# Optimization experiments

Measured on AMD Instinct MI355X. Metric: run time of the kernel, lower is better.

## Reference

```python
import jax, jax.numpy as jnp
import numpy as np

STATE_LEN = 128
SEQ_LEN = 2048  # middle segment length; total T = SEQ_LEN + 2*STATE_LEN = 2304


def _l2norm(t):
    # matches torch F.normalize(p=2, dim=-1, eps=1e-12)
    n = jnp.sqrt(jnp.sum(t * t, axis=-1, keepdims=True))
    return t / jnp.maximum(n, 1e-12)


def setup_inputs() -> dict:
    key = jax.random.key(0)
    ks = jax.random.split(key, 8)
    B, D, H, dk, dv = 1, 1024, 16, 64, 64
    T = SEQ_LEN + 2 * STATE_LEN
    x = jax.random.normal(ks[0], (B, T, D), dtype=jnp.float32)
    w = lambda k, do: jax.random.normal(k, (H, D, do), dtype=jnp.float32) * 0.02
    return {
        "x": x,
        "Wq": w(ks[1], dk),
        "Wk": w(ks[2], dk),
        "Wv": w(ks[3], dv),
        "Wq_state": w(ks[4], dk),
        "Wk_state": w(ks[5], dk),
        "Wv_state": w(ks[6], dv),
        "scaling_factor": jnp.full((H,), 1.0 / np.sqrt(dk), dtype=jnp.float32),
    }


def reference(x, Wq, Wk, Wv, Wq_state, Wk_state, Wv_state, scaling_factor):
    sl, seq = STATE_LEN, SEQ_LEN
    # extract_state: [start_state | sequence | end_state]
    x0 = x[:, :sl]
    xm = x[:, sl:sl + seq]
    x1 = x[:, sl + seq:]

    proj = lambda t, W: jnp.einsum('bsd,hdk->bhsk', t, W)  # StackedLinear, no bias

    q = jnp.concatenate([_l2norm(proj(x0, Wq_state)), _l2norm(proj(xm, Wq)), _l2norm(proj(x1, Wq_state))], axis=2)
    k = jnp.concatenate([_l2norm(proj(x0, Wk_state)), _l2norm(proj(xm, Wk)), _l2norm(proj(x1, Wk_state))], axis=2)
    v = jnp.concatenate([_l2norm(proj(x0, Wv_state)), _l2norm(proj(xm, Wv)), _l2norm(proj(x1, Wv_state))], axis=2)

    T = q.shape[2]
    row = jnp.arange(T)[:, None]
    col = jnp.arange(T)[None, :]
    allowed = col <= row  # causal (tril, diagonal=0)
    # end-state rows may not attend to start-state cols (attn_bias[..., seq+sl:seq+2sl, :sl] = 0 before log)
    allowed = allowed & ~((row >= sl + seq) & (col < sl))
    mask = jnp.where(allowed, 0.0, -jnp.inf).astype(q.dtype)  # log of 0/1 tril

    # per-head learnable scale applied to q@k^T, then additive mask, softmax, @v
    scores = jnp.einsum('bhqd,bhkd->bhqk', q, k) * scaling_factor[None, :, None, None] + mask
    att = jax.nn.softmax(scores, axis=-1)
    return jnp.einsum('bhqk,bhkd->bhqd', att, v)
```

## Files before the change

kernel.cpp:

```cpp
#include <hip/hip_runtime.h>
#include <hip/hip_bf16.h>

#define T_TOT 2304
#define DDIM  1024
#define NH    16
#define DK    64
#define SLEN  128
#define SEQ   2048

typedef __bf16 bf16x8 __attribute__((ext_vector_type(8)));
typedef __bf16 bf16x4 __attribute__((ext_vector_type(4)));
typedef float  f32x4  __attribute__((ext_vector_type(4)));
typedef float  f32x16 __attribute__((ext_vector_type(16)));

__device__ __forceinline__ void async_copy16(const void* gsrc, void* ldst) {
  __builtin_amdgcn_global_load_lds(
      (const __attribute__((address_space(1))) void*)gsrc,
      (__attribute__((address_space(3))) void*)ldst, 16, 0, 0);
}

__device__ __forceinline__ void lds_barrier() {
  __asm__ volatile("s_waitcnt lgkmcnt(0)\n\ts_barrier" ::: "memory");
}

__global__ __launch_bounds__(256) void convert_kernel(
    const float* __restrict__ x,
    const float* __restrict__ Wq, const float* __restrict__ Wk,
    const float* __restrict__ Wv, const float* __restrict__ Wqs,
    const float* __restrict__ Wks, const float* __restrict__ Wvs,
    __bf16* __restrict__ xb, __bf16* __restrict__ Wt) {
  const int b = blockIdx.x;
  const int tid = threadIdx.x;
  if (b < 576) {
    const float4* xin = (const float4*)x;
#pragma unroll
    for (int it = 0; it < 4; ++it) {
      int idx4 = b * 1024 + it * 256 + tid;
      float4 v = xin[idx4];
      bf16x4 o;
      o[0] = (__bf16)v.x; o[1] = (__bf16)v.y; o[2] = (__bf16)v.z; o[3] = (__bf16)v.w;
      *(bf16x4*)(xb + (size_t)idx4 * 4) = o;
    }
    return;
  }
  __shared__ float tile[64 * 65];
  const int wb = b - 576;
  const int m  = wb >> 8;
  const int rem = wb & 255;
  const int h  = rem >> 4;
  const int dt = rem & 15;
  const int d0 = dt * 64;
  const float* Wsrc = (m == 0 ? Wq : m == 1 ? Wk : m == 2 ? Wv
                      : m == 3 ? Wqs : m == 4 ? Wks : Wvs) + (size_t)h * (DDIM * DK);
#pragma unroll
  for (int rr = 0; rr < 4; ++rr) {
    int drow = rr * 16 + (tid >> 4);
    int nc   = (tid & 15) * 4;
    float4 v = *(const float4*)(Wsrc + (size_t)(d0 + drow) * DK + nc);
    tile[(nc + 0) * 65 + drow] = v.x;
    tile[(nc + 1) * 65 + drow] = v.y;
    tile[(nc + 2) * 65 + drow] = v.z;
    tile[(nc + 3) * 65 + drow] = v.w;
  }
  __syncthreads();
  {
    int n  = tid >> 2;
    int rg = (tid & 3) * 16;
    __bf16* dst = Wt + (((size_t)(m * NH + h)) * DK + n) * DDIM + d0 + rg;
    bf16x8 o0, o1;
#pragma unroll
    for (int e = 0; e < 8; e++) o0[e] = (__bf16)tile[n * 65 + rg + e];
#pragma unroll
    for (int e = 0; e < 8; e++) o1[e] = (__bf16)tile[n * 65 + rg + 8 + e];
    *(bf16x8*)dst = o0;
    *(bf16x8*)(dst + 8) = o1;
  }
}

__global__ __launch_bounds__(256) void proj_kernel(
    const __bf16* __restrict__ xb, const __bf16* __restrict__ Wt,
    const float* __restrict__ scal,
    __bf16* __restrict__ qkv, __bf16* __restrict__ vt) {
  const int ntile = blockIdx.x;
  const int rt    = blockIdx.y;
  const int which = blockIdx.z;
  const int r0    = rt * 128;
  const int m     = (rt == 0 || rt == 17) ? which + 3 : which;

  __shared__ __bf16 Xs[128 * 64];
  __shared__ __bf16 Wsh[128 * 64];

  const int tid  = threadIdx.x;
  const int wave = tid >> 6, lane = tid & 63;
  const int quad = lane >> 4, lc = lane & 15;
  const int wr   = wave >> 1, wc = wave & 1;
  const int h    = ntile * 2 + wc;

  const __bf16* Wbase = Wt + ((size_t)m * NH) * (DK * DDIM) + (size_t)(ntile * 128) * DDIM;

  const f32x4 fz = {0.f, 0.f, 0.f, 0.f};
  f32x4 acc[4][4];
#pragma unroll
  for (int i = 0; i < 4; i++)
#pragma unroll
    for (int j = 0; j < 4; j++) acc[i][j] = fz;

  for (int k0 = 0; k0 < DDIM; k0 += 64) {
#pragma unroll
    for (int it = 0; it < 4; ++it) {
      int L = it * 256 + tid;
      int row = L >> 3, c = (L & 7) ^ ((L >> 3) & 7);
      async_copy16(xb + (size_t)(r0 + row) * DDIM + k0 + c * 8,
                   (char*)Xs + (size_t)(it * 256 + wave * 64) * 16);
    }
#pragma unroll
    for (int it = 0; it < 4; ++it) {
      int L = it * 256 + tid;
      int row = L >> 3, c = (L & 7) ^ ((L >> 3) & 7);
      async_copy16(Wbase + (size_t)row * DDIM + k0 + c * 8,
                   (char*)Wsh + (size_t)(it * 256 + wave * 64) * 16);
    }
    __syncthreads();
#pragma unroll
    for (int kk = 0; kk < 2; kk++) {
      bf16x8 afr[4], bfr[4];
#pragma unroll
      for (int i = 0; i < 4; i++) {
        int row = wr * 64 + i * 16 + lc;
        int ch  = (kk * 4 + quad) ^ (row & 7);
        afr[i] = *(const bf16x8*)(Xs + (row * 8 + ch) * 8);
      }
#pragma unroll
      for (int j = 0; j < 4; j++) {
        int row = wc * 64 + j * 16 + lc;
        int ch  = (kk * 4 + quad) ^ (row & 7);
        bfr[j] = *(const bf16x8*)(Wsh + (row * 8 + ch) * 8);
      }
#pragma unroll
      for (int i = 0; i < 4; i++)
#pragma unroll
        for (int j = 0; j < 4; j++)
          acc[i][j] = __builtin_amdgcn_mfma_f32_16x16x32_bf16(afr[i], bfr[j], acc[i][j], 0, 0, 0);
    }
    __syncthreads();
  }

  const float qscale = (which == 0) ? scal[h] * 1.44269504088896f : 1.0f;
  float inv4[4][4];
#pragma unroll
  for (int i = 0; i < 4; i++) {
#pragma unroll
    for (int r = 0; r < 4; r++) {
      float s = 0.f;
#pragma unroll
      for (int j = 0; j < 4; j++) { float v = acc[i][j][r]; s += v * v; }
#pragma unroll
      for (int off = 1; off < 16; off <<= 1) s += __shfl_xor(s, off, 64);
      inv4[i][r] = qscale / fmaxf(sqrtf(s), 1e-12f);
    }
  }
  if (which == 2) {
    __bf16* vtp = vt + (size_t)h * (DK * T_TOT);
#pragma unroll
    for (int i = 0; i < 4; i++) {
      int rowbase = r0 + wr * 64 + i * 16 + quad * 4;
#pragma unroll
      for (int j = 0; j < 4; j++) {
        bf16x4 o;
#pragma unroll
        for (int r = 0; r < 4; r++) o[r] = (__bf16)(acc[i][j][r] * inv4[i][r]);
        *(bf16x4*)(vtp + (size_t)(j * 16 + lc) * T_TOT + rowbase) = o;
      }
    }
  } else {
    __bf16* outp = qkv + ((size_t)(which * NH + h)) * ((size_t)T_TOT * DK);
#pragma unroll
    for (int i = 0; i < 4; i++)
#pragma unroll
      for (int r = 0; r < 4; r++) {
        int row = r0 + wr * 64 + i * 16 + quad * 4 + r;
#pragma unroll
        for (int j = 0; j < 4; j++)
          outp[(size_t)row * DK + j * 16 + lc] = (__bf16)(acc[i][j][r] * inv4[i][r]);
      }
  }
}

__global__ __launch_bounds__(256, 3) void attn_kernel(
    const __bf16* __restrict__ qkv, const __bf16* __restrict__ vt,
    float* __restrict__ out) {
  const int b    = blockIdx.x;
  const int h    = b & 15;
  const int qg   = 35 - (b >> 4);
  const int q0b  = qg * 64;
  const int tid  = threadIdx.x;
  const int wave = tid >> 6, lane = tid & 63;
  const int quad = lane >> 4, lc = lane & 15;
  const int l32  = lane & 31, hi = lane >> 5;

  const __bf16* qp = qkv + ((size_t)h) * ((size_t)T_TOT * DK);
  const __bf16* kp = qkv + ((size_t)(NH + h)) * ((size_t)T_TOT * DK);
  const __bf16* vp = vt + (size_t)h * (DK * T_TOT);

  __shared__ __bf16 Ks[2][64 * 64];
  __shared__ __bf16 Vs[2][64 * 64];
  __shared__ __bf16 Ps[64 * 64];
  __shared__ float  lred[4][64];

  bf16x8 qf[4][2];
#pragma unroll
  for (int qt = 0; qt < 4; qt++)
#pragma unroll
    for (int kk = 0; kk < 2; kk++)
      qf[qt][kk] = *(const bf16x8*)(qp + (size_t)(q0b + qt * 16 + lc) * DK + kk * 32 + quad * 8);

  f32x16 acc_o;
#pragma unroll
  for (int e = 0; e < 16; e++) acc_o[e] = 0.f;
  float lp[4] = {0.f, 0.f, 0.f, 0.f};

  const int jstart = (q0b >= SLEN + SEQ) ? 2 : 0;
  const int jend   = qg;

  auto stage = [&](int j, int bufi) {
    const __bf16* kT = kp + (size_t)j * 64 * DK;
#pragma unroll
    for (int it = 0; it < 2; ++it) {
      int L = it * 256 + tid;
      int row = L >> 3, c = (L & 7) ^ ((L >> 3) & 7);
      async_copy16(kT + (size_t)row * DK + c * 8,
                   (char*)&Ks[bufi][0] + (size_t)(it * 256 + wave * 64) * 16);
    }
#pragma unroll
    for (int it = 0; it < 2; ++it) {
      int L = it * 256 + tid;
      int d = L >> 3, c = (L & 7) ^ ((L >> 3) & 7);
      async_copy16(vp + (size_t)d * T_TOT + j * 64 + c * 8,
                   (char*)&Vs[bufi][0] + (size_t)(it * 256 + wave * 64) * 16);
    }
  };

  stage(jstart, 0);
  int cur = 0;

  const int d0 = (wave >> 1) * 32;
  const int q0 = (wave & 1) * 32;

  for (int j = jstart; j <= jend; ++j) {
    __syncthreads();
    if (j < jend) stage(j + 1, cur ^ 1);

    const bool diag = (j == jend);

    bf16x8 kA[2];
#pragma unroll
    for (int kk = 0; kk < 2; kk++) {
      int row = wave * 16 + lc;
      kA[kk] = *(const bf16x8*)(&Ks[cur][(row * 8 + ((kk * 4 + quad) ^ (lc & 7))) * 8]);
    }
    f32x4 s[4];
#pragma unroll
    for (int qt = 0; qt < 4; qt++) {
      s[qt] = (f32x4){0.f, 0.f, 0.f, 0.f};
#pragma unroll
      for (int kk = 0; kk < 2; kk++)
        s[qt] = __builtin_amdgcn_mfma_f32_16x16x32_bf16(kA[kk], qf[qt][kk], s[qt], 0, 0, 0);
    }

#pragma unroll
    for (int qt = 0; qt < 4; qt++) {
      if (diag) {
#pragma unroll
        for (int r = 0; r < 4; r++)
          if ((wave * 16 + quad * 4 + r) > (qt * 16 + lc)) s[qt][r] = -__builtin_inff();
      }
      bf16x4 pb;
#pragma unroll
      for (int r = 0; r < 4; r++) {
        float pe = exp2f(s[qt][r]);
        lp[qt] += pe;
        pb[r] = (__bf16)pe;
      }
      int el = (qt * 16 + lc) * 64 + (((wave * 2 + (quad >> 1)) ^ (lc & 7)) * 8) + (quad & 1) * 4;
      *(bf16x4*)(&Ps[el]) = pb;
    }

    lds_barrier();

#pragma unroll
    for (int ks = 0; ks < 4; ks++) {
      int ch = (ks * 2 + hi) ^ (l32 & 7);
      bf16x8 vA = *(const bf16x8*)(&Vs[cur][((d0 + l32) * 8 + ch) * 8]);
      bf16x8 pB = *(const bf16x8*)(&Ps[((q0 + l32) * 8 + ch) * 8]);
      acc_o = __builtin_amdgcn_mfma_f32_32x32x16_bf16(vA, pB, acc_o, 0, 0, 0);
    }
    cur ^= 1;
  }

#pragma unroll
  for (int qt = 0; qt < 4; qt++) {
    lp[qt] += __shfl_xor(lp[qt], 16, 64);
    lp[qt] += __shfl_xor(lp[qt], 32, 64);
  }
  lred[wave][quad * 16 + lc] = lp[quad];
  __syncthreads();
  float lsum = lred[0][q0 + l32] + lred[1][q0 + l32] + lred[2][q0 + l32] + lred[3][q0 + l32];
  float invl = 1.0f / lsum;

  const size_t rowbase = ((size_t)h * T_TOT + q0b + q0 + l32) * DK;
#pragma unroll
  for (int g = 0; g < 4; g++) {
    f32x4 o;
#pragma unroll
    for (int t = 0; t < 4; t++) o[t] = acc_o[g * 4 + t] * invl;
    *(f32x4*)(&out[rowbase + d0 + 4 * hi + 8 * g]) = o;
  }
}

extern "C" void kernel_launch(void* const* d_in, const int* in_sizes, int n_in,
                              void* d_out, int out_size, void* d_ws, size_t ws_size,
                              hipStream_t stream) {
  const float* x    = (const float*)d_in[0];
  const float* Wq   = (const float*)d_in[1];
  const float* Wk   = (const float*)d_in[2];
  const float* Wv   = (const float*)d_in[3];
  const float* Wqs  = (const float*)d_in[4];
  const float* Wks  = (const float*)d_in[5];
  const float* Wvs  = (const float*)d_in[6];
  const float* scal = (const float*)d_in[7];
  float* out = (float*)d_out;

  char* ws = (char*)d_ws;
  size_t off = 0;
  __bf16* xb  = (__bf16*)(ws + off); off += (size_t)T_TOT * DDIM * 2;
  __bf16* Wt  = (__bf16*)(ws + off); off += (size_t)6 * NH * DK * DDIM * 2;
  __bf16* qkv = (__bf16*)(ws + off); off += (size_t)2 * NH * T_TOT * DK * 2;
  __bf16* vt  = (__bf16*)(ws + off);

  convert_kernel<<<2112, 256, 0, stream>>>(x, Wq, Wk, Wv, Wqs, Wks, Wvs, xb, Wt);
  proj_kernel<<<dim3(8, 18, 3), 256, 0, stream>>>(xb, Wt, scal, qkv, vt);
  attn_kernel<<<dim3(576), 256, 0, stream>>>(qkv, vt, out);
}
```

Before: 155.7 us.

## Split attention key range across two blocks and add combine kernel

Each query tile's causal key range is split into two halves processed by separate blocks, which write unnormalized partial outputs and row sums to workspace. A new combine kernel sums the two partials and normalizes. This doubles the grid and shortens the longest per-block loop to reduce causal load imbalance. In exchange it adds partial-result memory traffic and an extra kernel launch.

New measurement: 148.5 us. 1.05x faster.

```diff
diff --git a/kernel.cpp b/kernel.cpp
--- a/kernel.cpp
+++ b/kernel.cpp
@@ -188,10 +188,12 @@
 
 __global__ __launch_bounds__(256, 3) void attn_kernel(
     const __bf16* __restrict__ qkv, const __bf16* __restrict__ vt,
-    float* __restrict__ out) {
+    float* __restrict__ Opart, float* __restrict__ Lpart) {
   const int b    = blockIdx.x;
   const int h    = b & 15;
-  const int qg   = 35 - (b >> 4);
+  const int rest = b >> 4;
+  const int qg   = 35 - (rest >> 1);
+  const int si   = rest & 1;
   const int q0b  = qg * 64;
   const int tid  = threadIdx.x;
   const int wave = tid >> 6, lane = tid & 63;
@@ -219,8 +221,11 @@
   for (int e = 0; e < 16; e++) acc_o[e] = 0.f;
   float lp[4] = {0.f, 0.f, 0.f, 0.f};
 
-  const int jstart = (q0b >= SLEN + SEQ) ? 2 : 0;
-  const int jend   = qg;
+  const int jsAll = (q0b >= SLEN + SEQ) ? 2 : 0;
+  const int n     = qg - jsAll + 1;
+  const int half  = (n + 1) >> 1;
+  const int j0    = jsAll + (si ? half : 0);
+  const int j1    = si ? qg : (jsAll + half - 1);
 
   auto stage = [&](int j, int bufi) {
     const __bf16* kT = kp + (size_t)j * 64 * DK;
@@ -240,17 +245,17 @@
     }
   };
 
-  stage(jstart, 0);
   int cur = 0;
+  if (j0 <= j1) stage(j0, 0);
 
   const int d0 = (wave >> 1) * 32;
   const int q0 = (wave & 1) * 32;
 
-  for (int j = jstart; j <= jend; ++j) {
+  for (int j = j0; j <= j1; ++j) {
     __syncthreads();
-    if (j < jend) stage(j + 1, cur ^ 1);
-
-    const bool diag = (j == jend);
+    if (j < j1) stage(j + 1, cur ^ 1);
+
+    const bool diag = (j == qg);
 
     bf16x8 kA[2];
 #pragma unroll
@@ -304,16 +309,48 @@
   }
   lred[wave][quad * 16 + lc] = lp[quad];
   __syncthreads();
-  float lsum = lred[0][q0 + l32] + lred[1][q0 + l32] + lred[2][q0 + l32] + lred[3][q0 + l32];
-  float invl = 1.0f / lsum;
-
-  const size_t rowbase = ((size_t)h * T_TOT + q0b + q0 + l32) * DK;
+  if (wave == 0)
+    Lpart[(size_t)b * 64 + lane] = lred[0][lane] + lred[1][lane] + lred[2][lane] + lred[3][lane];
+
+  float* Ob = Opart + (size_t)b * 4096;
+  const size_t rowbase = (size_t)(q0 + l32) * DK;
 #pragma unroll
   for (int g = 0; g < 4; g++) {
     f32x4 o;
 #pragma unroll
-    for (int t = 0; t < 4; t++) o[t] = acc_o[g * 4 + t] * invl;
-    *(f32x4*)(&out[rowbase + d0 + 4 * hi + 8 * g]) = o;
+    for (int t = 0; t < 4; t++) o[t] = acc_o[g * 4 + t];
+    *(f32x4*)(&Ob[rowbase + d0 + 4 * hi + 8 * g]) = o;
+  }
+}
+
+__global__ __launch_bounds__(256) void combine_kernel(
+    const float* __restrict__ Opart, const float* __restrict__ Lpart,
+    float* __restrict__ out) {
+  const int b  = blockIdx.x;
+  const int h  = b & 15;
+  const int qg = b >> 4;
+  const int b0 = (((35 - qg) * 2) << 4) | h;
+  const int b1 = b0 + 16;
+  const int tid = threadIdx.x;
+
+  __shared__ float invl[64];
+  if (tid < 64)
+    invl[tid] = 1.0f / (Lpart[(size_t)b0 * 64 + tid] + Lpart[(size_t)b1 * 64 + tid]);
+  __syncthreads();
+
+  const float* O0 = Opart + (size_t)b0 * 4096;
+  const float* O1 = Opart + (size_t)b1 * 4096;
+  float* op = out + ((size_t)h * T_TOT + qg * 64) * DK;
+#pragma unroll
+  for (int it = 0; it < 4; ++it) {
+    int i4 = it * 256 + tid;
+    f32x4 a = *(const f32x4*)(&O0[i4 * 4]);
+    f32x4 c = *(const f32x4*)(&O1[i4 * 4]);
+    float iv = invl[i4 >> 4];
+    f32x4 o;
+#pragma unroll
+    for (int r = 0; r < 4; r++) o[r] = (a[r] + c[r]) * iv;
+    *(f32x4*)(&op[i4 * 4]) = o;
   }
 }
 
@@ -332,12 +369,15 @@
 
   char* ws = (char*)d_ws;
   size_t off = 0;
-  __bf16* xb  = (__bf16*)(ws + off); off += (size_t)T_TOT * DDIM * 2;
-  __bf16* Wt  = (__bf16*)(ws + off); off += (size_t)6 * NH * DK * DDIM * 2;
-  __bf16* qkv = (__bf16*)(ws + off); off += (size_t)2 * NH * T_TOT * DK * 2;
-  __bf16* vt  = (__bf16*)(ws + off);
+  __bf16* xb    = (__bf16*)(ws + off); off += (size_t)T_TOT * DDIM * 2;
+  __bf16* Wt    = (__bf16*)(ws + off); off += (size_t)6 * NH * DK * DDIM * 2;
+  __bf16* qkv   = (__bf16*)(ws + off); off += (size_t)2 * NH * T_TOT * DK * 2;
+  __bf16* vt    = (__bf16*)(ws + off); off += (size_t)NH * DK * T_TOT * 2;
+  float*  Opart = (float*)(ws + off);  off += (size_t)1152 * 4096 * 4;
+  float*  Lpart = (float*)(ws + off);
 
   convert_kernel<<<2112, 256, 0, stream>>>(x, Wq, Wk, Wv, Wqs, Wks, Wvs, xb, Wt);
   proj_kernel<<<dim3(8, 18, 3), 256, 0, stream>>>(xb, Wt, scal, qkv, vt);
-  attn_kernel<<<dim3(576), 256, 0, stream>>>(qkv, vt, out);
-}
+  attn_kernel<<<dim3(1152), 256, 0, stream>>>(qkv, vt, Opart, Lpart);
+  combine_kernel<<<dim3(576), 256, 0, stream>>>(Opart, Lpart, out);
+}
```
